# Kernel optimization log

Measured on AMD Instinct MI355X. Metric: run time of the kernel, lower is better.

## Reference

```python
import jax, jax.numpy as jnp
import numpy as np

TOP_K = 8
N_GROUPS = 8
TOP_K_GROUPS = 4
ROUTE_SCALE = 2.5


def setup_inputs() -> dict:
    key = jax.random.key(0)
    k1, k2, k3 = jax.random.split(key, 3)
    x = jax.random.normal(k1, (8192, 7168), dtype=jnp.float32)
    weight = jax.random.normal(k2, (256, 7168), dtype=jnp.float32) * 0.02
    bias = jax.random.normal(k3, (256,), dtype=jnp.float32) * 0.1
    return {"x": x, "weight": weight, "bias": bias}


def reference(x, weight, bias):
    n_tokens = x.shape[0]
    n_experts = weight.shape[0]
    # scores: [T, E]
    logits = jnp.einsum('td,ed->te', x, weight)
    scores = jax.nn.sigmoid(logits)
    original_scores = scores
    scores_b = scores + bias  # bias branch (dim == 7168)
    # group-limited routing
    sg = scores_b.reshape(n_tokens, N_GROUPS, n_experts // N_GROUPS)
    # bias is not None -> group score = sum of top-2 within group
    top2, _ = jax.lax.top_k(sg, 2)
    group_scores = top2.sum(axis=-1)  # [T, G]
    _, group_idx = jax.lax.top_k(group_scores, TOP_K_GROUPS)  # [T, Kg]
    keep = jnp.zeros((n_tokens, N_GROUPS), dtype=bool)
    keep = keep.at[jnp.arange(n_tokens)[:, None], group_idx].set(True)
    masked = jnp.where(keep[:, :, None], sg, -jnp.inf).reshape(n_tokens, n_experts)
    # global top-k over masked scores
    _, indices = jax.lax.top_k(masked, TOP_K)  # [T, K]
    weights = jnp.take_along_axis(original_scores, indices, axis=1)
    weights = weights / weights.sum(axis=-1, keepdims=True)  # sigmoid normalization
    weights = weights * ROUTE_SCALE
    return weights.astype(x.dtype), indices
```

## Files before the change

### kernel.cpp

```cpp
#include <hip/hip_runtime.h>
#include <math.h>

#define T_TOKENS 8192
#define NEXP 256
#define DIM 7168
#define NSPLIT 4
#define KSPL (DIM / NSPLIT)
#define NITER (KSPL / 32)
#define NEG_INF (-3.0e38f)

typedef _Float16 f16;
typedef _Float16 f16x8 __attribute__((ext_vector_type(8)));
typedef __fp16 h16x2 __attribute__((ext_vector_type(2)));
typedef float f32x4 __attribute__((ext_vector_type(4)));
typedef float f32x16 __attribute__((ext_vector_type(16)));

#define AS1 __attribute__((address_space(1)))
#define AS3 __attribute__((address_space(3)))

#define WTILED_BYTES (2 * NEXP * DIM * 2)
#define PART_OFF WTILED_BYTES
#define UNSCALE 5.9604644775390625e-8f
#define STG 49152

__global__ __launch_bounds__(256) void wconvert(const float* __restrict__ w,
                                                char* __restrict__ wt) {
    const int n = blockIdx.x * 256 + threadIdx.x;
    const int K8 = n % 896;
    const int e = n / 896;
    const f32x4 u0 = *(const f32x4*)(w + (size_t)e * DIM + K8 * 8);
    const f32x4 u1 = *(const f32x4*)(w + (size_t)e * DIM + K8 * 8 + 4);
    float c[8] = {u0[0]*4096.f, u0[1]*4096.f, u0[2]*4096.f, u0[3]*4096.f,
                  u1[0]*4096.f, u1[1]*4096.f, u1[2]*4096.f, u1[3]*4096.f};
    f16x8 h, g;
#pragma unroll
    for (int j = 0; j < 4; ++j) {
        h16x2 hp = __builtin_amdgcn_cvt_pkrtz(c[2*j], c[2*j+1]);
        float r0 = c[2*j]   - (float)hp[0];
        float r1 = c[2*j+1] - (float)hp[1];
        h16x2 gp = __builtin_amdgcn_cvt_pkrtz(r0, r1);
        h[2*j] = (f16)hp[0]; h[2*j+1] = (f16)hp[1];
        g[2*j] = (f16)gp[0]; g[2*j+1] = (f16)gp[1];
    }
    const int T = K8 >> 2;
    const int kk = (K8 >> 1) & 1;
    const int lhi = K8 & 1;
    const int ntg = e >> 5, l31 = e & 31;
    char* base = wt + (size_t)T * 32768 + ntg * 1024 + lhi * 512 + l31 * 16;
    *(f16x8*)(base + (kk * 2 + 0) * 8192) = h;
    *(f16x8*)(base + (kk * 2 + 1) * 8192) = g;
}

__global__ __launch_bounds__(512, 2) void gemm32x(
    const float* __restrict__ x, const char* __restrict__ wt,
    float* __restrict__ part) {
    extern __shared__ __align__(16) char smem[];
    const int tid = threadIdx.x;
    const int lane = tid & 63;
    const int wv = tid >> 6;
    const int bm = blockIdx.x, bz = blockIdx.y;
    const int wr = wv >> 2, wcn = wv & 3;
    const int l31 = lane & 31, lhi = lane >> 5;

    const char* xc = (const char*)x;

    int aoff[2], ldsA[2];
#pragma unroll
    for (int i = 0; i < 2; ++i) {
        const int u = wv * 2 + i;
        const int ra = u * 8 + (lane >> 3);
        const int ua = lane & 7;
        aoff[i] = (bm * 128 + ra) * (DIM * 4) + bz * (KSPL * 4)
                + ((ua ^ (ra & 7)) * 16);
        ldsA[i] = u * 1024;
    }
    const char* wbase = wt + (size_t)bz * NITER * 32768;
    int woff[4], ldsW[4];
#pragma unroll
    for (int i = 0; i < 4; ++i) {
        const int u = wv * 4 + i;
        woff[i] = u * 1024 + lane * 16;
        ldsW[i] = 16384 + u * 1024;
    }

    int rA[2][2][2];
#pragma unroll
    for (int mt = 0; mt < 2; ++mt)
#pragma unroll
        for (int kk = 0; kk < 2; ++kk) {
            const int row = wr * 64 + mt * 32 + l31;
#pragma unroll
            for (int i = 0; i < 2; ++i) {
                const int u = kk * 4 + lhi * 2 + i;
                rA[mt][kk][i] = row * 128 + ((u ^ (row & 7)) * 16);
            }
        }
    int rW[2][2][2];
#pragma unroll
    for (int kk = 0; kk < 2; ++kk)
#pragma unroll
        for (int p = 0; p < 2; ++p)
#pragma unroll
            for (int ntl = 0; ntl < 2; ++ntl)
                rW[kk][p][ntl] = 16384 + ((kk * 2 + p) * 8 + wcn * 2 + ntl) * 1024
                               + lhi * 512 + l31 * 16;

    f32x16 acc[2][2];
#pragma unroll
    for (int mt = 0; mt < 2; ++mt)
#pragma unroll
        for (int ntl = 0; ntl < 2; ++ntl)
#pragma unroll
            for (int r = 0; r < 16; ++r) acc[mt][ntl][r] = 0.0f;

#define STAGE(sb)                                                               \
    {                                                                           \
        _Pragma("unroll")                                                       \
        for (int i = 0; i < 2; ++i)                                             \
            __builtin_amdgcn_global_load_lds((const AS1 void*)(xc + aoff[i]),   \
                (AS3 void*)(smem + (sb) + ldsA[i]), 16, 0, 0);                  \
        _Pragma("unroll")                                                       \
        for (int i = 0; i < 4; ++i)                                             \
            __builtin_amdgcn_global_load_lds((const AS1 void*)(wbase + woff[i]),\
                (AS3 void*)(smem + (sb) + ldsW[i]), 16, 0, 0);                  \
        _Pragma("unroll")                                                       \
        for (int i = 0; i < 2; ++i) aoff[i] += 128;                             \
        _Pragma("unroll")                                                       \
        for (int i = 0; i < 4; ++i) woff[i] += 32768;                           \
    }

#define COMPUTE(cb)                                                             \
    {                                                                           \
        _Pragma("unroll")                                                       \
        for (int kk = 0; kk < 2; ++kk) {                                        \
            f16x8 wb[2][2];                                                     \
            _Pragma("unroll")                                                   \
            for (int p = 0; p < 2; ++p)                                         \
                _Pragma("unroll")                                               \
                for (int ntl = 0; ntl < 2; ++ntl)                               \
                    wb[p][ntl] = *(const f16x8*)(smem + (cb) + rW[kk][p][ntl]); \
            f16x8 a0[2], a1[2];                                                 \
            _Pragma("unroll")                                                   \
            for (int mt = 0; mt < 2; ++mt) {                                    \
                const f32x4 v0 = *(const f32x4*)(smem + (cb) + rA[mt][kk][0]);  \
                const f32x4 v1 = *(const f32x4*)(smem + (cb) + rA[mt][kk][1]);  \
                float c[8] = {v0[0]*4096.f, v0[1]*4096.f, v0[2]*4096.f, v0[3]*4096.f,\
                              v1[0]*4096.f, v1[1]*4096.f, v1[2]*4096.f, v1[3]*4096.f};\
                _Pragma("unroll")                                               \
                for (int j = 0; j < 4; ++j) {                                   \
                    h16x2 hp = __builtin_amdgcn_cvt_pkrtz(c[2*j], c[2*j+1]);    \
                    float r0 = c[2*j]   - (float)hp[0];                         \
                    float r1 = c[2*j+1] - (float)hp[1];                         \
                    h16x2 gp = __builtin_amdgcn_cvt_pkrtz(r0, r1);              \
                    a0[mt][2*j] = (f16)hp[0]; a0[mt][2*j+1] = (f16)hp[1];       \
                    a1[mt][2*j] = (f16)gp[0]; a1[mt][2*j+1] = (f16)gp[1];       \
                }                                                               \
            }                                                                   \
            __builtin_amdgcn_s_setprio(1);                                      \
            _Pragma("unroll")                                                   \
            for (int mt = 0; mt < 2; ++mt)                                      \
                _Pragma("unroll")                                               \
                for (int ntl = 0; ntl < 2; ++ntl) {                             \
                    acc[mt][ntl] = __builtin_amdgcn_mfma_f32_32x32x16_f16(a0[mt], wb[0][ntl], acc[mt][ntl], 0, 0, 0); \
                    acc[mt][ntl] = __builtin_amdgcn_mfma_f32_32x32x16_f16(a1[mt], wb[0][ntl], acc[mt][ntl], 0, 0, 0); \
                    acc[mt][ntl] = __builtin_amdgcn_mfma_f32_32x32x16_f16(a0[mt], wb[1][ntl], acc[mt][ntl], 0, 0, 0); \
                    acc[mt][ntl] = __builtin_amdgcn_mfma_f32_32x32x16_f16(a1[mt], wb[1][ntl], acc[mt][ntl], 0, 0, 0); \
                }                                                               \
            __builtin_amdgcn_s_setprio(0);                                      \
        }                                                                       \
    }

    STAGE(0);
    STAGE(STG);
    int cb = 0;
    int nb = 2 * STG;
    for (int t = 0; t < NITER - 2; ++t) {
        STAGE(nb);
        asm volatile("s_waitcnt vmcnt(12)" ::: "memory");
        __builtin_amdgcn_sched_barrier(0);
        __builtin_amdgcn_s_barrier();
        COMPUTE(cb);
        __builtin_amdgcn_s_barrier();
        const int ob = cb;
        cb = (cb == 2 * STG) ? 0 : cb + STG;
        nb = ob;
    }
    asm volatile("s_waitcnt vmcnt(6)" ::: "memory");
    __builtin_amdgcn_sched_barrier(0);
    __builtin_amdgcn_s_barrier();
    COMPUTE(cb);
    __builtin_amdgcn_s_barrier();
    cb = (cb == 2 * STG) ? 0 : cb + STG;
    asm volatile("s_waitcnt vmcnt(0)" ::: "memory");
    __builtin_amdgcn_sched_barrier(0);
    __builtin_amdgcn_s_barrier();
    COMPUTE(cb);
#undef STAGE
#undef COMPUTE

    float* P = part + (size_t)bz * T_TOKENS * NEXP;
#pragma unroll
    for (int mt = 0; mt < 2; ++mt)
#pragma unroll
        for (int ntl = 0; ntl < 2; ++ntl) {
            const int gcol = (wcn * 2 + ntl) * 32 + l31;
#pragma unroll
            for (int r = 0; r < 16; ++r) {
                const int row32 = (r & 3) + 8 * (r >> 2) + 4 * lhi;
                const int grow = bm * 128 + wr * 64 + mt * 32 + row32;
                P[(size_t)grow * NEXP + gcol] = acc[mt][ntl][r];
            }
        }
}

__global__ __launch_bounds__(256) void routing_kernel(const float* __restrict__ part,
                                                      const float* __restrict__ bias,
                                                      float* __restrict__ out) {
    const int lane = threadIdx.x & 63;
    const int t = blockIdx.x * 4 + (threadIdx.x >> 6);

    f32x4 z = {0.f, 0.f, 0.f, 0.f};
#pragma unroll
    for (int s = 0; s < NSPLIT; ++s) {
        const f32x4 v = *((const f32x4*)(part + ((size_t)s * T_TOKENS + t) * NEXP) + lane);
        z[0] += v[0]; z[1] += v[1]; z[2] += v[2]; z[3] += v[3];
    }
    const float s0 = 1.0f / (1.0f + expf(-z[0] * UNSCALE));
    const float s1 = 1.0f / (1.0f + expf(-z[1] * UNSCALE));
    const float s2 = 1.0f / (1.0f + expf(-z[2] * UNSCALE));
    const float s3 = 1.0f / (1.0f + expf(-z[3] * UNSCALE));
    const f32x4 bv = *((const f32x4*)bias + lane);
    float sb0 = s0 + bv[0], sb1 = s1 + bv[1], sb2 = s2 + bv[2], sb3 = s3 + bv[3];

    float m1, m2;
    m1 = sb0; m2 = NEG_INF;
    if (sb1 > m1) { m2 = m1; m1 = sb1; } else if (sb1 > m2) m2 = sb1;
    if (sb2 > m1) { m2 = m1; m1 = sb2; } else if (sb2 > m2) m2 = sb2;
    if (sb3 > m1) { m2 = m1; m1 = sb3; } else if (sb3 > m2) m2 = sb3;
#pragma unroll
    for (int off = 1; off < 8; off <<= 1) {
        const float om1 = __shfl_xor(m1, off);
        const float om2 = __shfl_xor(m2, off);
        const float hi = fmaxf(m1, om1);
        const float lo = fminf(m1, om1);
        m2 = fmaxf(lo, fmaxf(m2, om2));
        m1 = hi;
    }
    const float gs = m1 + m2;

    const float g0 = __shfl(gs, 0),  g1 = __shfl(gs, 8),  g2 = __shfl(gs, 16), g3 = __shfl(gs, 24);
    const float g4 = __shfl(gs, 32), g5 = __shfl(gs, 40), g6 = __shfl(gs, 48), g7 = __shfl(gs, 56);

    float t1 = NEG_INF, t2 = NEG_INF, t3 = NEG_INF, t4 = NEG_INF;
    int i1 = 0, i2 = 0, i3 = 0, i4 = 0;
#define INS4(v, gi)                                                         \
    {                                                                       \
        if (v > t1)      { t4=t3;i4=i3; t3=t2;i3=i2; t2=t1;i2=i1; t1=v;i1=gi; } \
        else if (v > t2) { t4=t3;i4=i3; t3=t2;i3=i2; t2=v;i2=gi; }          \
        else if (v > t3) { t4=t3;i4=i3; t3=v;i3=gi; }                       \
        else if (v > t4) { t4=v;i4=gi; }                                    \
    }
    INS4(g0, 0) INS4(g1, 1) INS4(g2, 2) INS4(g3, 3)
    INS4(g4, 4) INS4(g5, 5) INS4(g6, 6) INS4(g7, 7)
#undef INS4
    const int keepmask = (1 << i1) | (1 << i2) | (1 << i3) | (1 << i4);

    const int g = lane >> 3;
    if (!((keepmask >> g) & 1)) { sb0 = NEG_INF; sb1 = NEG_INF; sb2 = NEG_INF; sb3 = NEG_INF; }

    float wval[8];
    int wi[8];
    float wsum = 0.0f;
#pragma unroll
    for (int r = 0; r < 8; r++) {
        float bvv = sb0;
        int bii = (lane << 2);
        if (sb1 > bvv) { bvv = sb1; bii = (lane << 2) | 1; }
        if (sb2 > bvv) { bvv = sb2; bii = (lane << 2) | 2; }
        if (sb3 > bvv) { bvv = sb3; bii = (lane << 2) | 3; }
#pragma unroll
        for (int off = 1; off < 64; off <<= 1) {
            const float ov = __shfl_xor(bvv, off);
            const int oi = __shfl_xor(bii, off);
            if (ov > bvv || (ov == bvv && oi < bii)) { bvv = ov; bii = oi; }
        }
        const int sl = bii & 3;
        const float cand = (sl == 0) ? s0 : (sl == 1) ? s1 : (sl == 2) ? s2 : s3;
        const float ow = __shfl(cand, bii >> 2);
        wval[r] = ow;
        wi[r] = bii;
        wsum += ow;
        if ((bii >> 2) == lane) {
            if (sl == 0) sb0 = NEG_INF;
            else if (sl == 1) sb1 = NEG_INF;
            else if (sl == 2) sb2 = NEG_INF;
            else sb3 = NEG_INF;
        }
    }
    const float scale = 2.5f / wsum;
    if (lane == 0) {
        float* ow8 = out + (size_t)t * 8;
        float* oi8 = out + (size_t)T_TOKENS * 8 + (size_t)t * 8;
#pragma unroll
        for (int r = 0; r < 8; r++) {
            ow8[r] = wval[r] * scale;
            oi8[r] = (float)wi[r];
        }
    }
}

extern "C" void kernel_launch(void* const* d_in, const int* in_sizes, int n_in,
                              void* d_out, int out_size, void* d_ws, size_t ws_size,
                              hipStream_t stream) {
    const float* x = (const float*)d_in[0];
    const float* w = (const float*)d_in[1];
    const float* bias = (const float*)d_in[2];

    char* wt = (char*)d_ws;
    float* part = (float*)((char*)d_ws + PART_OFF);

    (void)hipFuncSetAttribute((const void*)gemm32x,
                              hipFuncAttributeMaxDynamicSharedMemorySize, 3 * STG);

    wconvert<<<NEXP * DIM / (256 * 8), 256, 0, stream>>>(w, wt);
    gemm32x<<<dim3(64, NSPLIT), 512, 3 * STG, stream>>>(x, wt, part);
    routing_kernel<<<T_TOKENS / 4, 256, 0, stream>>>(part, bias, (float*)d_out);
}
```

Before: 154.2 us.

## Load weight fragments directly to registers and remap blocks across XCDs

The GEMM stops staging the tiled fp16 weights through LDS. Each wave now loads its own 32-expert weight slice straight into registers, double-buffered one iteration ahead, and computes all 128 rows of the block. Only the x tile goes through LDS, which cuts LDS from 48KB to 16KB per stage. Blocks are linearized and remapped so that blocks sharing a K-split land on the same XCD, for L2 locality. The cost is that each wave converts all four row tiles of fp32 x to split fp16, so the conversion work is no longer shared across waves, and register pressure rises.

```diff
diff --git a/kernel.cpp b/kernel.cpp
--- a/kernel.cpp
+++ b/kernel.cpp
@@ -17,11 +17,12 @@
 
 #define AS1 __attribute__((address_space(1)))
 #define AS3 __attribute__((address_space(3)))
+typedef const AS1 f16x8* gf16x8p;
 
 #define WTILED_BYTES (2 * NEXP * DIM * 2)
 #define PART_OFF WTILED_BYTES
 #define UNSCALE 5.9604644775390625e-8f
-#define STG 49152
+#define STG 16384
 
 __global__ __launch_bounds__(256) void wconvert(const float* __restrict__ w,
                                                 char* __restrict__ wt) {
@@ -51,15 +52,17 @@
     *(f16x8*)(base + (kk * 2 + 1) * 8192) = g;
 }
 
-__global__ __launch_bounds__(512, 2) void gemm32x(
+__global__ __launch_bounds__(512, 2) void gemm32r(
     const float* __restrict__ x, const char* __restrict__ wt,
     float* __restrict__ part) {
-    extern __shared__ __align__(16) char smem[];
+    __shared__ char smem[3 * STG];
     const int tid = threadIdx.x;
     const int lane = tid & 63;
-    const int wv = tid >> 6;
-    const int bm = blockIdx.x, bz = blockIdx.y;
-    const int wr = wv >> 2, wcn = wv & 3;
+    const int wcn = tid >> 6;
+    const int b = blockIdx.x;
+    const int xcd = b & 7;
+    const int bz = xcd >> 1;
+    const int bm = (xcd & 1) * 32 + (b >> 3);
     const int l31 = lane & 31, lhi = lane >> 5;
 
     const char* xc = (const char*)x;
@@ -67,149 +70,117 @@
     int aoff[2], ldsA[2];
 #pragma unroll
     for (int i = 0; i < 2; ++i) {
-        const int u = wv * 2 + i;
+        const int u = wcn * 2 + i;
         const int ra = u * 8 + (lane >> 3);
         const int ua = lane & 7;
         aoff[i] = (bm * 128 + ra) * (DIM * 4) + bz * (KSPL * 4)
                 + ((ua ^ (ra & 7)) * 16);
         ldsA[i] = u * 1024;
     }
-    const char* wbase = wt + (size_t)bz * NITER * 32768;
-    int woff[4], ldsW[4];
-#pragma unroll
-    for (int i = 0; i < 4; ++i) {
-        const int u = wv * 4 + i;
-        woff[i] = u * 1024 + lane * 16;
-        ldsW[i] = 16384 + u * 1024;
-    }
-
-    int rA[2][2][2];
-#pragma unroll
-    for (int mt = 0; mt < 2; ++mt)
-#pragma unroll
-        for (int kk = 0; kk < 2; ++kk) {
-            const int row = wr * 64 + mt * 32 + l31;
-#pragma unroll
-            for (int i = 0; i < 2; ++i) {
-                const int u = kk * 4 + lhi * 2 + i;
-                rA[mt][kk][i] = row * 128 + ((u ^ (row & 7)) * 16);
-            }
-        }
-    int rW[2][2][2];
+    const AS1 char* wq = (const AS1 char*)(wt + (size_t)bz * NITER * 32768
+                                           + wcn * 1024 + lane * 16);
+
+    const int swz = l31 & 7;
+    int rbase[4], rx[2][2];
+#pragma unroll
+    for (int mt = 0; mt < 4; ++mt) rbase[mt] = (mt * 32 + l31) * 128;
 #pragma unroll
     for (int kk = 0; kk < 2; ++kk)
 #pragma unroll
-        for (int p = 0; p < 2; ++p)
-#pragma unroll
-            for (int ntl = 0; ntl < 2; ++ntl)
-                rW[kk][p][ntl] = 16384 + ((kk * 2 + p) * 8 + wcn * 2 + ntl) * 1024
-                               + lhi * 512 + l31 * 16;
-
-    f32x16 acc[2][2];
-#pragma unroll
-    for (int mt = 0; mt < 2; ++mt)
-#pragma unroll
-        for (int ntl = 0; ntl < 2; ++ntl)
-#pragma unroll
-            for (int r = 0; r < 16; ++r) acc[mt][ntl][r] = 0.0f;
-
-#define STAGE(sb)                                                               \
-    {                                                                           \
-        _Pragma("unroll")                                                       \
-        for (int i = 0; i < 2; ++i)                                             \
-            __builtin_amdgcn_global_load_lds((const AS1 void*)(xc + aoff[i]),   \
-                (AS3 void*)(smem + (sb) + ldsA[i]), 16, 0, 0);                  \
-        _Pragma("unroll")                                                       \
-        for (int i = 0; i < 4; ++i)                                             \
-            __builtin_amdgcn_global_load_lds((const AS1 void*)(wbase + woff[i]),\
-                (AS3 void*)(smem + (sb) + ldsW[i]), 16, 0, 0);                  \
-        _Pragma("unroll")                                                       \
-        for (int i = 0; i < 2; ++i) aoff[i] += 128;                             \
-        _Pragma("unroll")                                                       \
-        for (int i = 0; i < 4; ++i) woff[i] += 32768;                           \
-    }
-
-#define COMPUTE(cb)                                                             \
+        for (int i = 0; i < 2; ++i)
+            rx[kk][i] = ((kk * 4 + lhi * 2 + i) ^ swz) * 16;
+
+    f32x16 acc[4];
+#pragma unroll
+    for (int mt = 0; mt < 4; ++mt)
+#pragma unroll
+        for (int r = 0; r < 16; ++r) acc[mt][r] = 0.0f;
+
+    f16x8 wA[2][2], wB[2][2];
+
+#define COMPUTE(CB, W)                                                          \
     {                                                                           \
         _Pragma("unroll")                                                       \
         for (int kk = 0; kk < 2; ++kk) {                                        \
-            f16x8 wb[2][2];                                                     \
             _Pragma("unroll")                                                   \
-            for (int p = 0; p < 2; ++p)                                         \
-                _Pragma("unroll")                                               \
-                for (int ntl = 0; ntl < 2; ++ntl)                               \
-                    wb[p][ntl] = *(const f16x8*)(smem + (cb) + rW[kk][p][ntl]); \
-            f16x8 a0[2], a1[2];                                                 \
-            _Pragma("unroll")                                                   \
-            for (int mt = 0; mt < 2; ++mt) {                                    \
-                const f32x4 v0 = *(const f32x4*)(smem + (cb) + rA[mt][kk][0]);  \
-                const f32x4 v1 = *(const f32x4*)(smem + (cb) + rA[mt][kk][1]);  \
+            for (int mt = 0; mt < 4; ++mt) {                                    \
+                const f32x4 v0 = *(const f32x4*)(smem + (CB) + rbase[mt] + rx[kk][0]); \
+                const f32x4 v1 = *(const f32x4*)(smem + (CB) + rbase[mt] + rx[kk][1]); \
                 float c[8] = {v0[0]*4096.f, v0[1]*4096.f, v0[2]*4096.f, v0[3]*4096.f,\
                               v1[0]*4096.f, v1[1]*4096.f, v1[2]*4096.f, v1[3]*4096.f};\
+                f16x8 a0, a1;                                                   \
                 _Pragma("unroll")                                               \
                 for (int j = 0; j < 4; ++j) {                                   \
                     h16x2 hp = __builtin_amdgcn_cvt_pkrtz(c[2*j], c[2*j+1]);    \
                     float r0 = c[2*j]   - (float)hp[0];                         \
                     float r1 = c[2*j+1] - (float)hp[1];                         \
                     h16x2 gp = __builtin_amdgcn_cvt_pkrtz(r0, r1);              \
-                    a0[mt][2*j] = (f16)hp[0]; a0[mt][2*j+1] = (f16)hp[1];       \
-                    a1[mt][2*j] = (f16)gp[0]; a1[mt][2*j+1] = (f16)gp[1];       \
+                    a0[2*j] = (f16)hp[0]; a0[2*j+1] = (f16)hp[1];               \
+                    a1[2*j] = (f16)gp[0]; a1[2*j+1] = (f16)gp[1];               \
                 }                                                               \
+                __builtin_amdgcn_s_setprio(1);                                  \
+                acc[mt] = __builtin_amdgcn_mfma_f32_32x32x16_f16(a0, W[kk][0], acc[mt], 0, 0, 0); \
+                acc[mt] = __builtin_amdgcn_mfma_f32_32x32x16_f16(a1, W[kk][0], acc[mt], 0, 0, 0); \
+                acc[mt] = __builtin_amdgcn_mfma_f32_32x32x16_f16(a0, W[kk][1], acc[mt], 0, 0, 0); \
+                acc[mt] = __builtin_amdgcn_mfma_f32_32x32x16_f16(a1, W[kk][1], acc[mt], 0, 0, 0); \
+                __builtin_amdgcn_s_setprio(0);                                  \
             }                                                                   \
-            __builtin_amdgcn_s_setprio(1);                                      \
+        }                                                                       \
+    }
+
+#define BODY(T, WCUR, WNXT)                                                     \
+    {                                                                           \
+        const int kstage = ((T) + 2 < NITER) ? (T) + 2 : 0;                     \
+        _Pragma("unroll")                                                       \
+        for (int i = 0; i < 2; ++i)                                             \
+            __builtin_amdgcn_global_load_lds(                                   \
+                (const AS1 void*)(xc + aoff[i] + kstage * 128),                 \
+                (AS3 void*)(smem + nb + ldsA[i]), 16, 0, 0);                    \
+        const int kw = ((T) + 1 < NITER) ? (T) + 1 : 0;                         \
+        _Pragma("unroll")                                                       \
+        for (int kk = 0; kk < 2; ++kk)                                          \
             _Pragma("unroll")                                                   \
-            for (int mt = 0; mt < 2; ++mt)                                      \
-                _Pragma("unroll")                                               \
-                for (int ntl = 0; ntl < 2; ++ntl) {                             \
-                    acc[mt][ntl] = __builtin_amdgcn_mfma_f32_32x32x16_f16(a0[mt], wb[0][ntl], acc[mt][ntl], 0, 0, 0); \
-                    acc[mt][ntl] = __builtin_amdgcn_mfma_f32_32x32x16_f16(a1[mt], wb[0][ntl], acc[mt][ntl], 0, 0, 0); \
-                    acc[mt][ntl] = __builtin_amdgcn_mfma_f32_32x32x16_f16(a0[mt], wb[1][ntl], acc[mt][ntl], 0, 0, 0); \
-                    acc[mt][ntl] = __builtin_amdgcn_mfma_f32_32x32x16_f16(a1[mt], wb[1][ntl], acc[mt][ntl], 0, 0, 0); \
-                }                                                               \
-            __builtin_amdgcn_s_setprio(0);                                      \
-        }                                                                       \
-    }
-
-    STAGE(0);
-    STAGE(STG);
-    int cb = 0;
-    int nb = 2 * STG;
-    for (int t = 0; t < NITER - 2; ++t) {
-        STAGE(nb);
-        asm volatile("s_waitcnt vmcnt(12)" ::: "memory");
-        __builtin_amdgcn_sched_barrier(0);
-        __builtin_amdgcn_s_barrier();
-        COMPUTE(cb);
-        __builtin_amdgcn_s_barrier();
-        const int ob = cb;
-        cb = (cb == 2 * STG) ? 0 : cb + STG;
-        nb = ob;
-    }
-    asm volatile("s_waitcnt vmcnt(6)" ::: "memory");
-    __builtin_amdgcn_sched_barrier(0);
-    __builtin_amdgcn_s_barrier();
-    COMPUTE(cb);
-    __builtin_amdgcn_s_barrier();
-    cb = (cb == 2 * STG) ? 0 : cb + STG;
-    asm volatile("s_waitcnt vmcnt(0)" ::: "memory");
-    __builtin_amdgcn_sched_barrier(0);
-    __builtin_amdgcn_s_barrier();
-    COMPUTE(cb);
-#undef STAGE
+            for (int p = 0; p < 2; ++p)                                         \
+                WNXT[kk][p] = *(gf16x8p)(wq + (size_t)kw * 32768 + (kk * 2 + p) * 8192); \
+        asm volatile("s_waitcnt vmcnt(6)" ::: "memory");                        \
+        __builtin_amdgcn_sched_barrier(0);                                      \
+        __builtin_amdgcn_s_barrier();                                           \
+        COMPUTE(cb, WCUR);                                                      \
+        __builtin_amdgcn_s_barrier();                                           \
+        const int ob = cb; cb = (cb == 2 * STG) ? 0 : cb + STG; nb = ob;        \
+    }
+
+#pragma unroll
+    for (int i = 0; i < 2; ++i)
+        __builtin_amdgcn_global_load_lds((const AS1 void*)(xc + aoff[i]),
+                                         (AS3 void*)(smem + ldsA[i]), 16, 0, 0);
+#pragma unroll
+    for (int i = 0; i < 2; ++i)
+        __builtin_amdgcn_global_load_lds((const AS1 void*)(xc + aoff[i] + 128),
+                                         (AS3 void*)(smem + STG + ldsA[i]), 16, 0, 0);
+#pragma unroll
+    for (int kk = 0; kk < 2; ++kk)
+#pragma unroll
+        for (int p = 0; p < 2; ++p)
+            wA[kk][p] = *(gf16x8p)(wq + (kk * 2 + p) * 8192);
+
+    int cb = 0, nb = 2 * STG;
+    for (int tt = 0; tt < NITER; tt += 2) {
+        BODY(tt, wA, wB);
+        BODY(tt + 1, wB, wA);
+    }
+#undef BODY
 #undef COMPUTE
 
     float* P = part + (size_t)bz * T_TOKENS * NEXP;
-#pragma unroll
-    for (int mt = 0; mt < 2; ++mt)
-#pragma unroll
-        for (int ntl = 0; ntl < 2; ++ntl) {
-            const int gcol = (wcn * 2 + ntl) * 32 + l31;
-#pragma unroll
-            for (int r = 0; r < 16; ++r) {
-                const int row32 = (r & 3) + 8 * (r >> 2) + 4 * lhi;
-                const int grow = bm * 128 + wr * 64 + mt * 32 + row32;
-                P[(size_t)grow * NEXP + gcol] = acc[mt][ntl][r];
-            }
+    const int gcol = wcn * 32 + l31;
+#pragma unroll
+    for (int mt = 0; mt < 4; ++mt)
+#pragma unroll
+        for (int r = 0; r < 16; ++r) {
+            const int row32 = (r & 3) + 8 * (r >> 2) + 4 * lhi;
+            const int grow = bm * 128 + mt * 32 + row32;
+            P[(size_t)grow * NEXP + gcol] = acc[mt][r];
         }
 }
 
@@ -319,10 +290,7 @@
     char* wt = (char*)d_ws;
     float* part = (float*)((char*)d_ws + PART_OFF);
 
-    (void)hipFuncSetAttribute((const void*)gemm32x,
-                              hipFuncAttributeMaxDynamicSharedMemorySize, 3 * STG);
-
     wconvert<<<NEXP * DIM / (256 * 8), 256, 0, stream>>>(w, wt);
-    gemm32x<<<dim3(64, NSPLIT), 512, 3 * STG, stream>>>(x, wt, part);
+    gemm32r<<<256, 512, 0, stream>>>(x, wt, part);
     routing_kernel<<<T_TOKENS / 4, 256, 0, stream>>>(part, bias, (float*)d_out);
 }
```

New measurement: 164.8 us. +6.8%, slower.
